# Kernel optimization log

Hardware: AMD Instinct MI355X
Metric: run time of the kernel (lower is better)

The kernel has to match this reference:

```python
import math
import jax, jax.numpy as jnp
import numpy as np

H = 1024
NH = 16
HD = H // NH
FF = 4096


def gelu_erf(x):
    return x * 0.5 * (1.0 + jax.lax.erf(x / jnp.sqrt(jnp.float32(2.0))))


def layernorm(x, gamma, beta, eps=1e-12):
    mean = x.mean(axis=-1, keepdims=True)
    var = ((x - mean) ** 2).mean(axis=-1, keepdims=True)
    return gamma * (x - mean) / jnp.sqrt(var + eps) + beta


def setup_inputs() -> dict:
    key = jax.random.key(0)
    ks = jax.random.split(key, 12)
    B, S = 2, 2048
    sc = 0.02
    return {
        "x": jax.random.normal(ks[0], (B, S, H), jnp.float32),
        "attention_mask": jnp.ones((B, S), jnp.int32),
        "Wq": jax.random.normal(ks[1], (H, H), jnp.float32) * sc,
        "bq": jnp.zeros((H,), jnp.float32),
        "Wk": jax.random.normal(ks[2], (H, H), jnp.float32) * sc,
        "bk": jnp.zeros((H,), jnp.float32),
        "Wv": jax.random.normal(ks[3], (H, H), jnp.float32) * sc,
        "bv": jnp.zeros((H,), jnp.float32),
        "Wo": jax.random.normal(ks[4], (H, H), jnp.float32) * sc,
        "bo": jnp.zeros((H,), jnp.float32),
        "ln1_g": jnp.ones((H,), jnp.float32),
        "ln1_b": jnp.zeros((H,), jnp.float32),
        "W1": jax.random.normal(ks[5], (H, FF), jnp.float32) * sc,
        "b1": jnp.zeros((FF,), jnp.float32),
        "W2": jax.random.normal(ks[6], (FF, H), jnp.float32) * sc,
        "b2": jnp.zeros((H,), jnp.float32),
        "ln2_g": jnp.ones((H,), jnp.float32),
        "ln2_b": jnp.zeros((H,), jnp.float32),
    }


def reference(x, attention_mask, Wq, bq, Wk, bk, Wv, bv, Wo, bo,
              ln1_g, ln1_b, W1, b1, W2, b2, ln2_g, ln2_b):
    B, S, _ = x.shape
    # QKV projections, split heads -> [B, NH, S, HD]
    def split(t):
        return t.reshape(B, S, NH, HD).transpose(0, 2, 1, 3)
    q = split(x @ Wq + bq)
    k = split(x @ Wk + bk)
    v = split(x @ Wv + bv)
    # scores [B, NH, S, S]
    s = jnp.einsum("bhqd,bhkd->bhqk", q, k) / math.sqrt(HD)
    mask = (attention_mask == 1)[:, None, None, :]  # [B,1,1,S]
    s = jnp.where(mask, s, -jnp.inf)
    p = jax.nn.softmax(s, axis=-1)
    a = jnp.einsum("bhqk,bhkd->bhqd", p, v)
    a = a.transpose(0, 2, 1, 3).reshape(B, S, H)  # merge heads
    a = a @ Wo + bo
    a = layernorm(a, ln1_g, ln1_b)  # NOTE: no residual in source
    m = gelu_erf(a @ W1 + b1) @ W2 + b2
    return layernorm(m, ln2_g, ln2_b)
```

## Files before the change

### kernel.cpp

```cpp
#include <hip/hip_runtime.h>
#include <hip/hip_bf16.h>
#include <math.h>

typedef __bf16 bf16;
typedef __attribute__((ext_vector_type(8))) __bf16 bf16x8;
typedef __attribute__((ext_vector_type(4))) __bf16 bf16x4;
typedef __attribute__((ext_vector_type(2))) __bf16 bf16x2;
typedef __attribute__((ext_vector_type(4))) float f32x4;
typedef __attribute__((ext_vector_type(4))) short short4v;

#define HDIM 1024
#define NHEAD 16
#define HD 64
#define FFDIM 4096
#define BATCH 2
#define SEQ 2048
#define M_TOK 4096
#define NSPLIT 4
#define PSTRIDE ((size_t)M_TOK * HDIM)

static __device__ __forceinline__ void async_load16(const bf16* g, bf16* l) {
  __builtin_amdgcn_global_load_lds(
      (const __attribute__((address_space(1))) void*)g,
      (__attribute__((address_space(3))) void*)l, 16, 0, 0);
}

static __device__ __forceinline__ f32x4 mfma16_bf16(bf16x4 a, bf16x4 b, f32x4 c) {
#if defined(__HIP_DEVICE_COMPILE__)
#if __has_builtin(__builtin_amdgcn_mfma_f32_16x16x16bf16_1k)
  return __builtin_amdgcn_mfma_f32_16x16x16bf16_1k(
      __builtin_bit_cast(short4v, a), __builtin_bit_cast(short4v, b), c, 0, 0, 0);
#else
  return __builtin_amdgcn_mfma_f32_16x16x16_bf16(a, b, c, 0, 0, 0);
#endif
#else
  return c;
#endif
}

__global__ __launch_bounds__(256)
void prep_kernel(const float* __restrict__ x,
                 const float* __restrict__ Wq, const float* __restrict__ Wk,
                 const float* __restrict__ Wv, const float* __restrict__ Wo,
                 const float* __restrict__ W1, const float* __restrict__ W2,
                 bf16* __restrict__ Xb, bf16* __restrict__ QKVT,
                 bf16* __restrict__ W1T, bf16* __restrict__ W2T)
{
  const int z = blockIdx.z;
  const int t = threadIdx.x;
  if (z == 12) {
    const size_t base = ((size_t)(blockIdx.y * 32 + blockIdx.x)) * 4096;
#pragma unroll
    for (int j = 0; j < 4; ++j) {
      const size_t i = base + j * 1024 + t * 4;
      f32x4 v = *(const f32x4*)(x + i);
      bf16x4 o;
#pragma unroll
      for (int k = 0; k < 4; ++k) o[k] = (bf16)v[k];
      *(bf16x4*)(Xb + i) = o;
    }
    return;
  }
  const float* ps; bf16* pd; int sld, dld;
  if (z < 4) {
    ps = (z == 0) ? Wq : (z == 1) ? Wk : (z == 2) ? Wv : Wo;
    pd = QKVT + (size_t)z * HDIM * HDIM; sld = 1024; dld = 1024;
  } else if (z < 8) {
    const int c = z - 4;
    ps = W1 + c * 1024; sld = 4096;
    pd = W1T + (size_t)c * 1024 * 1024; dld = 1024;
  } else {
    const int c = z - 8;
    ps = W2 + (size_t)c * 1024 * 1024; sld = 1024;
    pd = W2T + c * 1024; dld = 4096;
  }
  __shared__ float tile[32][33];
  const int tx = t & 31, ty = t >> 5;
  const int c0 = blockIdx.x * 32, r0 = blockIdx.y * 32;
#pragma unroll
  for (int i = 0; i < 32; i += 8)
    tile[ty + i][tx] = ps[(size_t)(r0 + ty + i) * sld + c0 + tx];
  __syncthreads();
  const int rr0 = (t & 15) * 2;
  const int ccb = t >> 4;
#pragma unroll
  for (int i = 0; i < 2; ++i) {
    const int cc = ccb + 16 * i;
    bf16x2 v = {(bf16)tile[rr0][cc], (bf16)tile[rr0 + 1][cc]};
    *(bf16x2*)(pd + (size_t)(c0 + cc) * dld + r0 + rr0) = v;
  }
}

#define BSW(R, C) ((R) * 64 + ((C) ^ (((R) & 7) << 3)))

template<int EPI>
__global__ __launch_bounds__(256)
void gemm_bt(const bf16* __restrict__ A, const bf16* __restrict__ Bt,
             const float* __restrict__ b0, const float* __restrict__ b1p,
             const float* __restrict__ b2p, void* __restrict__ Cout,
             int M, int N, int ldk, int kchunk)
{
  __shared__ __align__(16) bf16 Smem[2][128 * 64];
  bf16* As = Smem[0];
  bf16* Bs = Smem[1];
  const int t = threadIdx.x;
  const int wave = t >> 6, lane = t & 63;
  const int lm = lane & 15, qd = lane >> 4;
  const int wm = (wave >> 1) * 64, wn = (wave & 1) * 64;

  const int nwg2d = gridDim.x * gridDim.y;
  const int cpx = nwg2d >> 3;
  const int lin2d = blockIdx.x + gridDim.x * blockIdx.y;
  const int swz = (lin2d & 7) * cpx + (lin2d >> 3);
  const int bxs = swz % gridDim.x;
  const int bys = swz / gridDim.x;
  const int bm = bys * 128, bn = bxs * 128;
  const int kbeg = blockIdx.z * kchunk;

  f32x4 acc[4][4] = {};
  const int srow = t >> 3;
  const int schk = t & 7;

  for (int k0 = kbeg; k0 < kbeg + kchunk; k0 += 64) {
#pragma unroll
    for (int r = 0; r < 4; ++r) {
      const int row = r * 32 + srow;
      const int chunk = schk ^ (row & 7);
      async_load16(A + (size_t)(bm + row) * ldk + (k0 + chunk * 8),
                   (bf16*)((char*)As + r * 4096 + t * 16));
    }
#pragma unroll
    for (int r = 0; r < 4; ++r) {
      const int row = r * 32 + srow;
      const int chunk = schk ^ (row & 7);
      async_load16(Bt + (size_t)(bn + row) * ldk + (k0 + chunk * 8),
                   (bf16*)((char*)Bs + r * 4096 + t * 16));
    }
    __syncthreads();
#pragma unroll
    for (int ks = 0; ks < 2; ++ks) {
      bf16x8 av[4], bv[4];
#pragma unroll
      for (int mt = 0; mt < 4; ++mt) {
        const int row = wm + mt * 16 + lm;
        const int chunk = (ks * 4 + qd) ^ (row & 7);
        av[mt] = *(const bf16x8*)(As + row * 64 + chunk * 8);
      }
#pragma unroll
      for (int nt = 0; nt < 4; ++nt) {
        const int row = wn + nt * 16 + lm;
        const int chunk = (ks * 4 + qd) ^ (row & 7);
        bv[nt] = *(const bf16x8*)(Bs + row * 64 + chunk * 8);
      }
#pragma unroll
      for (int mt = 0; mt < 4; ++mt)
#pragma unroll
        for (int nt = 0; nt < 4; ++nt)
          acc[mt][nt] = __builtin_amdgcn_mfma_f32_16x16x32_bf16(bv[nt], av[mt], acc[mt][nt], 0, 0, 0);
    }
    __syncthreads();
  }

  bf16* tw = &Smem[0][0] + wave * 4096;
  const bool vt = (EPI == 3) && ((bn + wn) >= 2 * HDIM);

#pragma unroll
  for (int nt = 0; nt < 4; ++nt) {
    const int n0 = bn + wn + nt * 16 + qd * 4;
    f32x4 bsv = {0.f, 0.f, 0.f, 0.f};
    if (EPI == 2) bsv = *(const f32x4*)(b0 + n0);
    if (EPI == 3) {
      const int sect = n0 >> 10, c = n0 & 1023;
      const float* bp = (sect == 0) ? b0 : (sect == 1) ? b1p : b2p;
      bsv = *(const f32x4*)(bp + c);
    }
#pragma unroll
    for (int mt = 0; mt < 4; ++mt) {
      f32x4 v;
#pragma unroll
      for (int r = 0; r < 4; ++r) v[r] = acc[mt][nt][r] + bsv[r];
      bf16x4 o;
      if (EPI == 2) {
#pragma unroll
        for (int r = 0; r < 4; ++r) {
          const float z = v[r] * 0.70710678118f;
          const float az = fabsf(z);
          const float tt = __builtin_amdgcn_rcpf(fmaf(az, 0.3275911f, 1.0f));
          const float poly = tt * fmaf(tt, fmaf(tt, fmaf(tt, fmaf(tt, 1.061405429f,
                             -1.453152027f), 1.421413741f), -0.284496736f), 0.254829592f);
          const float e = __builtin_amdgcn_exp2f(az * az * -1.4426950408889634f);
          float erfv = 1.0f - poly * e;
          erfv = (z < 0.f) ? -erfv : erfv;
          o[r] = (bf16)(0.5f * v[r] * (1.0f + erfv));
        }
      } else {
#pragma unroll
        for (int r = 0; r < 4; ++r) o[r] = (bf16)v[r];
      }
      if (!vt) {
        *(bf16x4*)(tw + BSW(mt * 16 + lm, nt * 16 + qd * 4)) = o;
      } else {
#pragma unroll
        for (int r = 0; r < 4; ++r)
          tw[BSW(nt * 16 + qd * 4 + r, mt * 16 + lm)] = o[r];
      }
    }
  }
  const int erow = lane >> 3, ech = lane & 7;
  if (EPI == 1) {
    bf16* dst = (bf16*)Cout + (size_t)blockIdx.z * M * N +
                (size_t)(bm + wm) * N + (bn + wn);
#pragma unroll
    for (int p = 0; p < 8; ++p) {
      const int row = p * 8 + erow;
      bf16x8 val = *(const bf16x8*)(tw + BSW(row, ech * 8));
      *(bf16x8*)(dst + (size_t)row * N + ech * 8) = val;
    }
  } else if (EPI == 2) {
    bf16* dst = (bf16*)Cout + (size_t)(bm + wm) * N + (bn + wn);
#pragma unroll
    for (int p = 0; p < 8; ++p) {
      const int row = p * 8 + erow;
      bf16x8 val = *(const bf16x8*)(tw + BSW(row, ech * 8));
      *(bf16x8*)(dst + (size_t)row * N + ech * 8) = val;
    }
  } else {
    bf16* base = (bf16*)Cout;
    const int sect = (bn + wn) >> 10;
    if (!vt) {
      bf16* dst = base + (size_t)sect * M_TOK * HDIM +
                  (size_t)(bm + wm) * HDIM + ((bn + wn) & 1023);
#pragma unroll
      for (int p = 0; p < 8; ++p) {
        const int row = p * 8 + erow;
        bf16x8 val = *(const bf16x8*)(tw + BSW(row, ech * 8));
        *(bf16x8*)(dst + (size_t)row * HDIM + ech * 8) = val;
      }
    } else {
      const int c0 = (bn + wn) & 1023;
      const int hh = c0 >> 6;
      const int bb = (bm + wm) >> 11, ss0 = (bm + wm) & 2047;
      bf16* dst = base + (size_t)2 * M_TOK * HDIM +
                  (size_t)((bb * NHEAD + hh) * HD) * SEQ + ss0;
#pragma unroll
      for (int p = 0; p < 8; ++p) {
        const int row = p * 8 + erow;
        bf16x8 val = *(const bf16x8*)(tw + BSW(row, ech * 8));
        *(bf16x8*)(dst + (size_t)row * SEQ + ech * 8) = val;
      }
    }
  }
}

__global__ __launch_bounds__(256)
void attn_kernel(const bf16* __restrict__ Q, const bf16* __restrict__ Kg,
                 const bf16* __restrict__ Vt, const int* __restrict__ mask,
                 bf16* __restrict__ Po, float* __restrict__ Lp)
{
  __shared__ __align__(16) bf16 Ks[64 * 64];
  __shared__ __align__(16) bf16 Vs[64 * 64];
  __shared__ float madd[64];

  const int t = threadIdx.x;
  const int wave = t >> 6, lane = t & 63;
  const int lm = lane & 15, qd = lane >> 4;

  const int lin = blockIdx.x;
  const int g = (lin & 7) * 16 + (lin >> 7);
  const int qblk = (lin >> 3) & 15;
  const int bh = g >> 2;
  const int split = g & 3;
  const int b = bh >> 4, h = bh & 15;
  const int q0 = qblk * 128 + wave * 32;
  const int kv_beg = split * (SEQ / NSPLIT);

  bf16x8 qf[2][2];
#pragma unroll
  for (int qt = 0; qt < 2; ++qt)
#pragma unroll
    for (int ks = 0; ks < 2; ++ks)
      qf[qt][ks] = *(const bf16x8*)(Q + (size_t)(b * SEQ + q0 + qt * 16 + lm) * HDIM +
                                    h * HD + ks * 32 + qd * 8);

  const bf16 onev = (bf16)1.0f;
  const bf16x4 ones = {onev, onev, onev, onev};
  f32x4 lacc[2] = {};
  f32x4 oacc[2][4] = {};

  const int srow = t >> 3, schk = t & 7;
  const float C = 0.1803368801f;

  for (int kv0 = kv_beg; kv0 < kv_beg + SEQ / NSPLIT; kv0 += 64) {
#pragma unroll
    for (int r = 0; r < 2; ++r) {
      const int row = r * 32 + srow;
      const int g2 = schk ^ (row & 7);
      async_load16(Kg + (size_t)(b * SEQ + kv0 + row) * HDIM + h * HD + g2 * 8,
                   (bf16*)((char*)Ks + r * 4096 + t * 16));
      async_load16(Vt + (size_t)(bh * HD + row) * SEQ + kv0 + g2 * 8,
                   (bf16*)((char*)Vs + r * 4096 + t * 16));
    }
    if (t < 64) madd[t] = (mask[b * SEQ + kv0 + t] == 1) ? 0.f : -1.0e30f;
    __syncthreads();

    bf16x8 kf[2][4];
#pragma unroll
    for (int ks = 0; ks < 2; ++ks)
#pragma unroll
      for (int nt = 0; nt < 4; ++nt) {
        const int row = nt * 16 + lm;
        const int c = (ks * 4 + qd) ^ (row & 7);
        kf[ks][nt] = *(const bf16x8*)(Ks + row * 64 + c * 8);
      }

    bf16x4 pf[2][4];
#pragma unroll
    for (int qt = 0; qt < 2; ++qt) {
      f32x4 sacc[4] = {};
#pragma unroll
      for (int ks = 0; ks < 2; ++ks)
#pragma unroll
        for (int nt = 0; nt < 4; ++nt)
          sacc[nt] = __builtin_amdgcn_mfma_f32_16x16x32_bf16(kf[ks][nt], qf[qt][ks], sacc[nt], 0, 0, 0);
#pragma unroll
      for (int nt = 0; nt < 4; ++nt) {
        f32x4 ma = *(const f32x4*)(madd + nt * 16 + qd * 4);
#pragma unroll
        for (int r = 0; r < 4; ++r)
          pf[qt][nt][r] = (bf16)__builtin_amdgcn_exp2f(fmaf(sacc[nt][r], C, ma[r]));
        lacc[qt] = mfma16_bf16(ones, pf[qt][nt], lacc[qt]);
      }
    }

#pragma unroll
    for (int nt2 = 0; nt2 < 4; ++nt2) {
      const int row = nt2 * 16 + lm;
#pragma unroll
      for (int nt = 0; nt < 4; ++nt) {
        bf16x4 vf = *(const bf16x4*)(Vs + row * 64 +
                     (((nt * 2 + (qd >> 1)) ^ (row & 7)) * 8) + (qd & 1) * 4);
        oacc[0][nt2] = mfma16_bf16(vf, pf[0][nt], oacc[0][nt2]);
        oacc[1][nt2] = mfma16_bf16(vf, pf[1][nt], oacc[1][nt2]);
      }
    }
    __syncthreads();
  }

  bf16* po = Po + (size_t)(split * 32 + bh) * 64 * SEQ;
#pragma unroll
  for (int qt = 0; qt < 2; ++qt) {
#pragma unroll
    for (int nt2 = 0; nt2 < 4; ++nt2)
#pragma unroll
      for (int r = 0; r < 4; ++r)
        po[(size_t)(nt2 * 16 + qd * 4 + r) * SEQ + q0 + qt * 16 + lm] =
            (bf16)oacc[qt][nt2][r];
    if (qd == 0)
      Lp[(size_t)(split * 32 + bh) * SEQ + q0 + qt * 16 + lm] = lacc[qt][0];
  }
}

__global__ __launch_bounds__(256)
void attn_merge(const bf16* __restrict__ Po, const float* __restrict__ Lp,
                bf16* __restrict__ Aout)
{
  __shared__ bf16 tile[64][80];
  __shared__ float linv[64];
  const int t = threadIdx.x;
  const int bh = blockIdx.y;
  const int b = bh >> 4, h = bh & 15;
  const int s0 = blockIdx.x * 64;

  if (t < 64) {
    float l = 0.f;
#pragma unroll
    for (int s = 0; s < NSPLIT; ++s)
      l += Lp[(size_t)(s * 32 + bh) * SEQ + s0 + t];
    linv[t] = 1.0f / l;
  }
  __syncthreads();

#pragma unroll
  for (int it = 0; it < 2; ++it) {
    const int d = (t >> 3) + 32 * it;
    const int sc = (t & 7) * 8;
    float acc[8] = {};
#pragma unroll
    for (int s = 0; s < NSPLIT; ++s) {
      bf16x8 v = *(const bf16x8*)(Po + ((size_t)(s * 32 + bh) * 64 + d) * SEQ + s0 + sc);
#pragma unroll
      for (int j = 0; j < 8; ++j) acc[j] += (float)v[j];
    }
#pragma unroll
    for (int j = 0; j < 8; ++j)
      tile[sc + j][d] = (bf16)(acc[j] * linv[sc + j]);
  }
  __syncthreads();

  const int tok = t >> 2, dc = (t & 3) * 16;
  bf16x8 o0 = *(const bf16x8*)&tile[tok][dc];
  bf16x8 o1 = *(const bf16x8*)&tile[tok][dc + 8];
  bf16* dst = Aout + (size_t)(b * SEQ + s0 + tok) * HDIM + h * HD + dc;
  *(bf16x8*)dst = o0;
  *(bf16x8*)(dst + 8) = o1;
}

template<int NP, int OUT_BF16>
__global__ __launch_bounds__(256)
void ln_sum(const bf16* __restrict__ p, const float* __restrict__ bias,
            const float* __restrict__ gamma, const float* __restrict__ beta,
            void* __restrict__ out)
{
  const int row = blockIdx.x;
  const int t = threadIdx.x;
  f32x4 v = {0.f, 0.f, 0.f, 0.f};
#pragma unroll
  for (int np = 0; np < NP; ++np) {
    bf16x4 u = *(const bf16x4*)(p + np * PSTRIDE + (size_t)row * HDIM + t * 4);
#pragma unroll
    for (int j = 0; j < 4; ++j) v[j] += (float)u[j];
  }
  f32x4 bv0 = *(const f32x4*)(bias + t * 4);
#pragma unroll
  for (int j = 0; j < 4; ++j) v[j] += bv0[j];

  float s = v[0] + v[1] + v[2] + v[3];
  float s2 = v[0] * v[0] + v[1] * v[1] + v[2] * v[2] + v[3] * v[3];
#pragma unroll
  for (int d = 1; d < 64; d <<= 1) { s += __shfl_xor(s, d, 64); s2 += __shfl_xor(s2, d, 64); }
  __shared__ float ss[4], ss2[4];
  const int wave = t >> 6, lane = t & 63;
  if (lane == 0) { ss[wave] = s; ss2[wave] = s2; }
  __syncthreads();
  s = ss[0] + ss[1] + ss[2] + ss[3];
  s2 = ss2[0] + ss2[1] + ss2[2] + ss2[3];
  const float mean = s * (1.0f / HDIM);
  const float var = s2 * (1.0f / HDIM) - mean * mean;
  const float rstd = rsqrtf(var + 1e-12f);
  f32x4 gv = *(const f32x4*)(gamma + t * 4);
  f32x4 bv = *(const f32x4*)(beta + t * 4);
  f32x4 y;
#pragma unroll
  for (int j = 0; j < 4; ++j) y[j] = gv[j] * (v[j] - mean) * rstd + bv[j];
  if (OUT_BF16) {
    bf16x4 o;
#pragma unroll
    for (int j = 0; j < 4; ++j) o[j] = (bf16)y[j];
    *(bf16x4*)((bf16*)out + (size_t)row * HDIM + t * 4) = o;
  } else {
    *(f32x4*)((float*)out + (size_t)row * HDIM + t * 4) = y;
  }
}

extern "C" void kernel_launch(void* const* d_in, const int* in_sizes, int n_in,
                              void* d_out, int out_size, void* d_ws, size_t ws_size,
                              hipStream_t stream)
{
  const float* x    = (const float*)d_in[0];
  const int*   am   = (const int*)d_in[1];
  const float* Wq   = (const float*)d_in[2];
  const float* bq   = (const float*)d_in[3];
  const float* Wk   = (const float*)d_in[4];
  const float* bk   = (const float*)d_in[5];
  const float* Wv   = (const float*)d_in[6];
  const float* bv   = (const float*)d_in[7];
  const float* Wo   = (const float*)d_in[8];
  const float* bo   = (const float*)d_in[9];
  const float* ln1g = (const float*)d_in[10];
  const float* ln1b = (const float*)d_in[11];
  const float* W1   = (const float*)d_in[12];
  const float* b1   = (const float*)d_in[13];
  const float* W2   = (const float*)d_in[14];
  const float* b2   = (const float*)d_in[15];
  const float* ln2g = (const float*)d_in[16];
  const float* ln2b = (const float*)d_in[17];

  char* ws = (char*)d_ws;
  const size_t MB = 1ull << 20;
  bf16*  W1T  = (bf16*)(ws + 0 * MB);
  bf16*  W2T  = (bf16*)(ws + 8 * MB);
  bf16*  Xb   = (bf16*)(ws + 16 * MB);
  bf16*  QKVT = (bf16*)(ws + 24 * MB);
  bf16*  WoT  = QKVT + (size_t)3 * HDIM * HDIM;
  bf16*  Qb   = (bf16*)(ws + 33 * MB);
  bf16*  Kb   = (bf16*)(ws + 41 * MB);
  bf16*  Vtb  = (bf16*)(ws + 49 * MB);
  bf16*  Po   = (bf16*)(ws + 57 * MB);
  float* Lp   = (float*)(ws + 89 * MB);
  bf16*  Ab   = (bf16*)(ws + 16 * MB);
  bf16*  Pw   = (bf16*)(ws + 33 * MB);
  bf16*  L1   = (bf16*)(ws + 65 * MB);
  bf16*  F1   = (bf16*)(ws + 16 * MB);
  bf16*  Pf   = (bf16*)(ws + 48 * MB);

  prep_kernel<<<dim3(32, 32, 13), 256, 0, stream>>>(x, Wq, Wk, Wv, Wo, W1, W2,
                                                    Xb, QKVT, W1T, W2T);

  gemm_bt<3><<<dim3(3072 / 128, M_TOK / 128, 1), 256, 0, stream>>>(
      Xb, QKVT, bq, bk, bv, Qb, M_TOK, 3072, HDIM, HDIM);

  attn_kernel<<<dim3(2048, 1, 1), 256, 0, stream>>>(Qb, Kb, Vtb, am, Po, Lp);
  attn_merge<<<dim3(SEQ / 64, BATCH * NHEAD), 256, 0, stream>>>(Po, Lp, Ab);

  gemm_bt<1><<<dim3(HDIM / 128, M_TOK / 128, 2), 256, 0, stream>>>(
      Ab, WoT, nullptr, nullptr, nullptr, Pw, M_TOK, HDIM, HDIM, 512);
  ln_sum<2, 1><<<M_TOK, 256, 0, stream>>>(Pw, bo, ln1g, ln1b, L1);

  gemm_bt<2><<<dim3(FFDIM / 128, M_TOK / 128, 1), 256, 0, stream>>>(
      L1, W1T, b1, nullptr, nullptr, F1, M_TOK, FFDIM, HDIM, HDIM);

  gemm_bt<1><<<dim3(HDIM / 128, M_TOK / 128, 4), 256, 0, stream>>>(
      F1, W2T, nullptr, nullptr, nullptr, Pf, M_TOK, HDIM, FFDIM, 1024);
  ln_sum<4, 0><<<M_TOK, 256, 0, stream>>>(Pf, b2, ln2g, ln2b, (float*)d_out);
}
```

Baseline: 345.2 us.

## Add 256x256-tile ping-pong GEMM kernel for FFN matmuls

```diff
diff --git a/kernel.cpp b/kernel.cpp
--- a/kernel.cpp
+++ b/kernel.cpp
@@ -36,6 +36,18 @@
 #else
   return c;
 #endif
+}
+
+static __device__ __forceinline__ float gelu_erf_f(float x) {
+  const float z = x * 0.70710678118f;
+  const float az = fabsf(z);
+  const float tt = __builtin_amdgcn_rcpf(fmaf(az, 0.3275911f, 1.0f));
+  const float poly = tt * fmaf(tt, fmaf(tt, fmaf(tt, fmaf(tt, 1.061405429f,
+                     -1.453152027f), 1.421413741f), -0.284496736f), 0.254829592f);
+  const float e = __builtin_amdgcn_exp2f(az * az * -1.4426950408889634f);
+  float erfv = 1.0f - poly * e;
+  erfv = (z < 0.f) ? -erfv : erfv;
+  return 0.5f * x * (1.0f + erfv);
 }
 
 __global__ __launch_bounds__(256)
@@ -182,17 +194,7 @@
       bf16x4 o;
       if (EPI == 2) {
 #pragma unroll
-        for (int r = 0; r < 4; ++r) {
-          const float z = v[r] * 0.70710678118f;
-          const float az = fabsf(z);
-          const float tt = __builtin_amdgcn_rcpf(fmaf(az, 0.3275911f, 1.0f));
-          const float poly = tt * fmaf(tt, fmaf(tt, fmaf(tt, fmaf(tt, 1.061405429f,
-                             -1.453152027f), 1.421413741f), -0.284496736f), 0.254829592f);
-          const float e = __builtin_amdgcn_exp2f(az * az * -1.4426950408889634f);
-          float erfv = 1.0f - poly * e;
-          erfv = (z < 0.f) ? -erfv : erfv;
-          o[r] = (bf16)(0.5f * v[r] * (1.0f + erfv));
-        }
+        for (int r = 0; r < 4; ++r) o[r] = (bf16)gelu_erf_f(v[r]);
       } else {
 #pragma unroll
         for (int r = 0; r < 4; ++r) o[r] = (bf16)v[r];
@@ -249,6 +251,166 @@
         *(bf16x8*)(dst + (size_t)row * SEQ + ech * 8) = val;
       }
     }
+  }
+}
+
+
+#define STAGE_Q(OP, BASEMN, LDSB, KOFF, Q) do { \
+    const int rr_ = (Q) * 64 + (t >> 3); \
+    const int gc_ = (t & 7) ^ (rr_ & 7); \
+    async_load16((OP) + (size_t)((BASEMN) + rr_) * ldk + (KOFF) + gc_ * 8, \
+                 (LDSB) + (Q) * 4096 + t * 8); \
+  } while (0)
+
+#define STAGE_HALF(OP, BASEMN, LDSB, KOFF, H) do { \
+    STAGE_Q(OP, BASEMN, LDSB, KOFF, 2 * (H)); \
+    STAGE_Q(OP, BASEMN, LDSB, KOFF, 2 * (H) + 1); \
+  } while (0)
+
+#define LOAD_AV(BUF, MH) do { \
+    _Pragma("unroll") \
+    for (int mt_ = 0; mt_ < 4; ++mt_) { \
+      const int row_ = wm + (MH) * 64 + mt_ * 16 + lm; \
+      _Pragma("unroll") \
+      for (int ks_ = 0; ks_ < 2; ++ks_) { \
+        const int c_ = (ks_ * 4 + qd) ^ (row_ & 7); \
+        av[mt_][ks_] = *(const bf16x8*)(As_[BUF] + row_ * 64 + c_ * 8); \
+      } \
+    } \
+  } while (0)
+
+#define LOAD_BV(DST, BUF, NH) do { \
+    _Pragma("unroll") \
+    for (int nt_ = 0; nt_ < 2; ++nt_) { \
+      const int row_ = wnb + (NH) * 32 + nt_ * 16 + lm; \
+      _Pragma("unroll") \
+      for (int ks_ = 0; ks_ < 2; ++ks_) { \
+        const int c_ = (ks_ * 4 + qd) ^ (row_ & 7); \
+        DST[nt_][ks_] = *(const bf16x8*)(Bs_[BUF] + row_ * 64 + c_ * 8); \
+      } \
+    } \
+  } while (0)
+
+#define MFMA_Q(MH, BV, NH) do { \
+    __builtin_amdgcn_s_setprio(1); \
+    _Pragma("unroll") \
+    for (int mt_ = 0; mt_ < 4; ++mt_) \
+      _Pragma("unroll") \
+      for (int nt_ = 0; nt_ < 2; ++nt_) \
+        _Pragma("unroll") \
+        for (int ks_ = 0; ks_ < 2; ++ks_) \
+          acc[(MH) * 4 + mt_][(NH) * 2 + nt_] = \
+              __builtin_amdgcn_mfma_f32_16x16x32_bf16( \
+                  BV[nt_][ks_], av[mt_][ks_], \
+                  acc[(MH) * 4 + mt_][(NH) * 2 + nt_], 0, 0, 0); \
+    __builtin_amdgcn_s_setprio(0); \
+  } while (0)
+
+#define SYNC_PRE() do { \
+    __builtin_amdgcn_s_barrier(); \
+    asm volatile("s_waitcnt lgkmcnt(0)" ::: "memory"); \
+    __builtin_amdgcn_sched_barrier(0); \
+  } while (0)
+#define SYNC_POST() do { \
+    __builtin_amdgcn_s_barrier(); \
+    __builtin_amdgcn_sched_barrier(0); \
+  } while (0)
+
+#define VMCNT4() asm volatile("s_waitcnt vmcnt(4)" ::: "memory")
+
+#define FOURPH(RB, WAB, KTA, WBB, KTB) do { \
+     \
+    LOAD_AV(RB, 0); LOAD_BV(bv0, RB, 0); \
+    STAGE_HALF(A, bm, As_[WAB], kbeg + (KTA) * 64, 0); \
+    SYNC_PRE(); MFMA_Q(0, bv0, 0); SYNC_POST(); \
+     \
+    LOAD_BV(bv1, RB, 1); \
+    STAGE_HALF(A, bm, As_[WAB], kbeg + (KTA) * 64, 1); \
+    SYNC_PRE(); MFMA_Q(0, bv1, 1); SYNC_POST(); \
+     \
+    LOAD_AV(RB, 1); \
+    STAGE_HALF(Bt, bn, Bs_[WBB], kbeg + (KTB) * 64, 0); \
+    SYNC_PRE(); MFMA_Q(1, bv0, 0); SYNC_POST(); \
+     \
+    STAGE_HALF(Bt, bn, Bs_[WBB], kbeg + (KTB) * 64, 1); \
+    SYNC_PRE(); MFMA_Q(1, bv1, 1); VMCNT4(); SYNC_POST(); \
+  } while (0)
+
+template<int EPI>
+__global__ __launch_bounds__(512, 2)
+void gemm256(const bf16* __restrict__ A, const bf16* __restrict__ Bt,
+             const float* __restrict__ b0, void* __restrict__ Cout,
+             int M, int N, int ldk, int kchunk)
+{
+  __shared__ __align__(16) bf16 SmemAll[4][256 * 64];
+  bf16* const As_[2] = {SmemAll[0], SmemAll[1]};
+  bf16* const Bs_[2] = {SmemAll[2], SmemAll[3]};
+
+  const int t = threadIdx.x;
+  const int wave = t >> 6, lane = t & 63;
+  const int lm = lane & 15, qd = lane >> 4;
+  const int wm = (wave >> 2) * 128;
+  const int wnb = (wave & 3) * 64;
+
+  const int nwg2d = gridDim.x * gridDim.y;
+  const int cpx = nwg2d >> 3;
+  const int lin2d = blockIdx.x + gridDim.x * blockIdx.y;
+  const int swz = (lin2d & 7) * cpx + (lin2d >> 3);
+  const int bm = (swz / gridDim.x) * 256, bn = (swz % gridDim.x) * 256;
+  const int kbeg = blockIdx.z * kchunk;
+  const int NT = kchunk >> 6;
+
+  f32x4 acc[8][4] = {};
+  bf16x8 av[4][2], bv0[2][2], bv1[2][2];
+
+  STAGE_HALF(Bt, bn, Bs_[0], kbeg, 0);
+  STAGE_HALF(Bt, bn, Bs_[0], kbeg, 1);
+  STAGE_HALF(A,  bm, As_[0], kbeg, 0);
+  STAGE_HALF(A,  bm, As_[0], kbeg, 1);
+  STAGE_HALF(Bt, bn, Bs_[1], kbeg + 64, 0);
+  STAGE_HALF(Bt, bn, Bs_[1], kbeg + 64, 1);
+  VMCNT4();
+  SYNC_POST();
+
+  for (int it = 0; it < NT / 2; ++it) {
+    const int tb = 2 * it + 1;
+    const int tc = (2 * it + 2) & (NT - 1);
+    const int td = (2 * it + 3) & (NT - 1);
+    FOURPH(0, 1, tb, 0, tc);
+    FOURPH(1, 0, tc, 1, td);
+  }
+
+  bf16* tw = &SmemAll[0][0] + wave * 8192;
+#pragma unroll
+  for (int nt4 = 0; nt4 < 4; ++nt4) {
+    const int n0 = bn + wnb + nt4 * 16 + qd * 4;
+    f32x4 bsv = {0.f, 0.f, 0.f, 0.f};
+    if (EPI == 2) bsv = *(const f32x4*)(b0 + n0);
+#pragma unroll
+    for (int mt8 = 0; mt8 < 8; ++mt8) {
+      f32x4 v;
+#pragma unroll
+      for (int r = 0; r < 4; ++r) v[r] = acc[mt8][nt4][r] + bsv[r];
+      bf16x4 o;
+      if (EPI == 2) {
+#pragma unroll
+        for (int r = 0; r < 4; ++r) o[r] = (bf16)gelu_erf_f(v[r]);
+      } else {
+#pragma unroll
+        for (int r = 0; r < 4; ++r) o[r] = (bf16)v[r];
+      }
+      *(bf16x4*)(tw + BSW(mt8 * 16 + lm, nt4 * 16 + qd * 4)) = o;
+    }
+  }
+  const int erow = lane >> 3, ech = lane & 7;
+  bf16* dst = (bf16*)Cout +
+              ((EPI == 1) ? (size_t)blockIdx.z * M * N : (size_t)0) +
+              (size_t)(bm + wm) * N + (bn + wnb);
+#pragma unroll
+  for (int p = 0; p < 16; ++p) {
+    const int row = p * 8 + erow;
+    bf16x8 val = *(const bf16x8*)(tw + BSW(row, ech * 8));
+    *(bf16x8*)(dst + (size_t)row * N + ech * 8) = val;
   }
 }
 
@@ -506,10 +668,10 @@
       Ab, WoT, nullptr, nullptr, nullptr, Pw, M_TOK, HDIM, HDIM, 512);
   ln_sum<2, 1><<<M_TOK, 256, 0, stream>>>(Pw, bo, ln1g, ln1b, L1);
 
-  gemm_bt<2><<<dim3(FFDIM / 128, M_TOK / 128, 1), 256, 0, stream>>>(
-      L1, W1T, b1, nullptr, nullptr, F1, M_TOK, FFDIM, HDIM, HDIM);
-
-  gemm_bt<1><<<dim3(HDIM / 128, M_TOK / 128, 4), 256, 0, stream>>>(
-      F1, W2T, nullptr, nullptr, nullptr, Pf, M_TOK, HDIM, FFDIM, 1024);
+  gemm256<2><<<dim3(FFDIM / 256, M_TOK / 256, 1), 512, 0, stream>>>(
+      L1, W1T, b1, F1, M_TOK, FFDIM, HDIM, HDIM);
+
+  gemm256<1><<<dim3(HDIM / 256, M_TOK / 256, 4), 512, 0, stream>>>(
+      F1, W2T, nullptr, Pf, M_TOK, HDIM, FFDIM, 1024);
   ln_sum<4, 0><<<M_TOK, 256, 0, stream>>>(Pf, b2, ln2g, ln2b, (float*)d_out);
 }
```

After: 336.7 us. 2.5% less time.
